# Kernel tuning notes

Hardware: AMD Instinct MI355X
Metric: run time of the kernel (lower is better)

## Reference

```python
import jax, jax.numpy as jnp
import numpy as np

B, K, D, H, L = 128, 128, 768, 8, 4
HD = D // H
FF = 4 * D
SIM = D // 4
BOOST = 0.3
SCALE = HD ** -0.5
EPS = 1e-5


def _ln(x, g, b):
    m = x.mean(-1, keepdims=True)
    v = ((x - m) ** 2).mean(-1, keepdims=True)
    return (x - m) * jax.lax.rsqrt(v + EPS) * g + b


def setup_inputs() -> dict:
    key = jax.random.key(0)
    ks = jax.random.split(key, 10)
    def n(k, shape, s=0.02):
        return jax.random.normal(k, shape, dtype=jnp.float32) * s
    return {
        'slots': jax.random.normal(ks[0], (B, K, D), dtype=jnp.float32),
        'pos_emb': n(ks[1], (1, K, D)),
        'Wq': n(ks[2], (L, D, D)),
        'Wk': n(ks[3], (L, D, D)),
        'Wv': n(ks[4], (L, D, D)),
        'Wo': n(ks[5], (L, D, D)),
        'bo': jnp.zeros((L, D), jnp.float32),
        'Wsim': n(ks[6], (L, D, SIM)),
        'g1': jnp.ones((L, D), jnp.float32),
        'b1': jnp.zeros((L, D), jnp.float32),
        'g2': jnp.ones((L, D), jnp.float32),
        'b2': jnp.zeros((L, D), jnp.float32),
        'Wff1': n(ks[7], (L, D, FF)),
        'bff1': jnp.zeros((L, FF), jnp.float32),
        'Wff2': n(ks[8], (L, FF, D)),
        'bff2': jnp.zeros((L, D), jnp.float32),
        'gf': jnp.ones((D,), jnp.float32),
        'bf': jnp.zeros((D,), jnp.float32),
    }


def reference(slots, pos_emb, Wq, Wk, Wv, Wo, bo, Wsim, g1, b1, g2, b2,
              Wff1, bff1, Wff2, bff2, gf, bf):
    x = slots + pos_emb  # K == max_slots -> full pos table
    for l in range(L):
        # --- similarity-biased multi-head self-attention (pre-norm) ---
        nx = _ln(x, g1[l], b1[l])
        q = (nx @ Wq[l]).reshape(B, K, H, HD)
        k = (nx @ Wk[l]).reshape(B, K, H, HD)
        v = (nx @ Wv[l]).reshape(B, K, H, HD)
        scores = jnp.einsum('bqhd,bkhd->bhqk', q, k) * SCALE  # [B,H,K,K]
        s = nx @ Wsim[l]  # [B,K,D/4]
        s = s / jnp.maximum(jnp.linalg.norm(s, axis=-1, keepdims=True), 1e-12)
        sim = jnp.einsum('bqc,bkc->bqk', s, s)  # cosine similarity matrix
        scores = scores + BOOST * sim[:, None, :, :]
        a = jax.nn.softmax(scores, axis=-1)
        o = jnp.einsum('bhqk,bkhd->bqhd', a, v).reshape(B, K, D)
        x = x + (o @ Wo[l] + bo[l])
        # --- feed-forward (pre-norm) ---
        nx = _ln(x, g2[l], b2[l])
        h = jax.nn.gelu(nx @ Wff1[l] + bff1[l], approximate=False)
        x = x + (h @ Wff2[l] + bff2[l])
    return _ln(x, gf, bf)
```

## Files before the change

kernel.cpp:

```cpp
#include <hip/hip_runtime.h>

typedef unsigned short u16;
typedef unsigned int u32;
typedef float f32x4 __attribute__((ext_vector_type(4)));
typedef __bf16 bf16x8 __attribute__((ext_vector_type(8)));

static constexpr int D = 768, FFD = 3072, SIMC = 192, NH = 8, HD = 96;
static constexpr int B = 128, K = 128, M = B * K, NL = 4;
static constexpr int QKVW = 2560;
static constexpr int SIMOFF = 2304;
static constexpr float QSCALE = 0.14724502f;
static constexpr float SBOOST2 = 0.6578821f;
static constexpr float EPS_F = 1e-5f;

__device__ __forceinline__ float bf2f(u16 u) {
  union { u32 i; float f; } v; v.i = ((u32)u) << 16; return v.f;
}
__device__ __forceinline__ u16 f2bf(float f) {
  union { float f; u32 i; } v; v.f = f;
  u32 u = v.i;
  u32 r = (u + 0x7FFFu + ((u >> 16) & 1u)) >> 16;
  return (u16)r;
}

__device__ __forceinline__ float fast_gelu(float x) {
  float u2 = x * (2.3020585f + 0.102944f * x * x);
  float e = __builtin_amdgcn_exp2f(u2);
  float r = __builtin_amdgcn_rcpf(1.0f + e);
  return x - x * r;
}

__device__ __forceinline__ void gload16(const void* g, void* l) {
  __builtin_amdgcn_global_load_lds(
      (const __attribute__((address_space(1))) void*)g,
      (__attribute__((address_space(3))) void*)l, 16, 0, 0);
}

__global__ __launch_bounds__(256) void addpos_kernel(
    const float* __restrict__ slots, const float* __restrict__ pos,
    u16* __restrict__ x) {
  int i = blockIdx.x * 256 + threadIdx.x;
  int m = i / D;
  int d = i - m * D;
  x[i] = f2bf(slots[i] + pos[(m & (K - 1)) * D + d]);
}

__device__ __forceinline__ float block_sum(float v, float* sbuf) {
#pragma unroll
  for (int off = 32; off > 0; off >>= 1) v += __shfl_xor(v, off, 64);
  int lane = threadIdx.x & 63, w = threadIdx.x >> 6;
  if (lane == 0) sbuf[w] = v;
  __syncthreads();
  v = sbuf[0] + sbuf[1] + sbuf[2] + sbuf[3];
  __syncthreads();
  return v;
}

template <bool OUT_BF16>
__global__ __launch_bounds__(256) void ln_kernel(
    const u16* __restrict__ x, const float* __restrict__ g,
    const float* __restrict__ b, void* __restrict__ out) {
  __shared__ float sbuf[4];
  int row = blockIdx.x, tid = threadIdx.x;
  const u16* xr = x + (size_t)row * D;
  float v0 = bf2f(xr[tid]), v1 = bf2f(xr[tid + 256]), v2 = bf2f(xr[tid + 512]);
  float s = block_sum(v0 + v1 + v2, sbuf);
  float mean = s * (1.0f / D);
  float d0 = v0 - mean, d1 = v1 - mean, d2 = v2 - mean;
  float sq = block_sum(d0 * d0 + d1 * d1 + d2 * d2, sbuf);
  float rs = rsqrtf(sq * (1.0f / D) + EPS_F);
  float y0 = d0 * rs * g[tid] + b[tid];
  float y1 = d1 * rs * g[tid + 256] + b[tid + 256];
  float y2 = d2 * rs * g[tid + 512] + b[tid + 512];
  if (OUT_BF16) {
    u16* o = (u16*)out + (size_t)row * D;
    o[tid] = f2bf(y0); o[tid + 256] = f2bf(y1); o[tid + 512] = f2bf(y2);
  } else {
    float* o = (float*)out + (size_t)row * D;
    o[tid] = y0; o[tid + 256] = y1; o[tid + 512] = y2;
  }
}

struct WAll {
  const float *wq, *wk, *wv, *wo, *wsim, *wff1, *wff2;
  u16 *tA, *tB, *tC, *tD;
};
__global__ __launch_bounds__(256) void wconv_all_kernel(WAll p, float qscale) {
  __shared__ u16 t[32][33];
  int bid = blockIdx.x;
  const float* W; u16* Wt; int N, Kd, n0, k0;
  float sc = 1.0f;
  if (bid < 2304) {
    int z = bid / 576, rem = bid - z * 576;
    W = z == 0 ? p.wq : z == 1 ? p.wk : z == 2 ? p.wv : p.wo;
    Wt = z == 0 ? p.tA : z == 1 ? p.tA + 768 * 768
       : z == 2 ? p.tA + 2 * 768 * 768 : p.tB;
    if (z == 0) sc = qscale;
    N = 768; Kd = 768;
    n0 = (rem % 24) * 32; k0 = (rem / 24) * 32;
  } else if (bid < 2448) {
    int rem = bid - 2304;
    W = p.wsim; Wt = p.tA + (size_t)SIMOFF * 768; N = SIMC; Kd = 768;
    n0 = (rem % 6) * 32; k0 = (rem / 6) * 32;
  } else if (bid < 4752) {
    int rem = bid - 2448;
    W = p.wff1; Wt = p.tC; N = FFD; Kd = 768;
    n0 = (rem % 96) * 32; k0 = (rem / 96) * 32;
  } else {
    int rem = bid - 4752;
    W = p.wff2; Wt = p.tD; N = 768; Kd = FFD;
    n0 = (rem % 24) * 32; k0 = (rem / 24) * 32;
  }
  int tid = threadIdx.x;
  int c = tid & 31, r4 = tid >> 5;
#pragma unroll
  for (int i = 0; i < 4; ++i) {
    int r = r4 + i * 8;
    t[r][c] = f2bf(W[(size_t)(k0 + r) * N + n0 + c] * sc);
  }
  __syncthreads();
#pragma unroll
  for (int i = 0; i < 4; ++i) {
    int r = r4 + i * 8;
    Wt[(size_t)(n0 + r) * Kd + k0 + c] = t[c][r];
  }
}

template <bool OUT_BF16, bool BIAS, bool GELU_, bool RESID>
__global__ __launch_bounds__(512, 2) void gemm256_kernel(
    const u16* __restrict__ A, const u16* __restrict__ Bt,
    const float* __restrict__ bias, const u16* __restrict__ resid,
    void* __restrict__ Cout, int N, int Kdim, int NBX) {
  __shared__ u16 lds[65536];
  int tid = threadIdx.x;
  int w = tid >> 6, lane = tid & 63;
  int wm = w >> 2, wn = w & 3;
  int lr = lane & 15, lg = lane >> 4;

  int nwg = gridDim.x;
  int cpx = nwg >> 3;
  int swz = (blockIdx.x & 7) * cpx + (blockIdx.x >> 3);
  int bx = swz % NBX, by = swz / NBX;
  int n0 = bx << 8, m0 = by << 8;

  int scol = ((lane & 7) ^ (lane >> 3)) << 3;
  size_t aOff = (size_t)((w << 4) + (lane >> 3)) * Kdim + scol;
  u16* ldsU = lds;

  auto stageA = [&](int buf, int h, int t) {
    const u16* g = A + (size_t)(m0 + (h << 7)) * Kdim + ((size_t)t << 6) + aOff;
    u16* l = ldsU + buf * 32768 + h * 8192 + (w << 10);
    gload16(g, l);
    gload16(g + ((size_t)Kdim << 3), l + 512);
  };
  auto stageB = [&](int buf, int h, int t) {
    const u16* g = Bt + (size_t)(n0 + (h << 7)) * Kdim + ((size_t)t << 6) + aOff;
    u16* l = ldsU + buf * 32768 + 16384 + h * 8192 + (w << 10);
    gload16(g, l);
    gload16(g + ((size_t)Kdim << 3), l + 512);
  };

  const u16* lA0p = ldsU;
  const u16* lB0p = ldsU + 16384;
  const u16* lA1p = ldsU + 32768;
  const u16* lB1p = ldsU + 49152;
  int arow = (wm * 128 + lr) * 64;
  int brow = (wn * 64 + lr) * 64;
  int swz0 = (((lg * 16)) ^ ((lr & 7) << 4)) >> 1;
  int swz1 = ((64 + lg * 16) ^ ((lr & 7) << 4)) >> 1;

  f32x4 acc[8][4] = {};
  bf16x8 ar[2][4], br[2][4];

#define READ_A_KS(BASE, MSEG, KS)                                            \
  do {                                                                       \
    _Pragma("unroll") for (int mm = 0; mm < 4; ++mm) {                       \
      const u16* p_ = (BASE) + arow + ((MSEG) * 64 + mm * 16) * 64;          \
      ar[KS][mm] = *(const bf16x8*)(p_ + ((KS) ? swz1 : swz0));              \
    }                                                                        \
  } while (0)
#define READ_B_KS(BASE, NSEG, KS)                                            \
  do {                                                                       \
    _Pragma("unroll") for (int nn = 0; nn < 2; ++nn) {                       \
      const u16* p_ = (BASE) + brow + ((NSEG) * 32 + nn * 16) * 64;          \
      br[KS][(NSEG) * 2 + nn] = *(const bf16x8*)(p_ + ((KS) ? swz1 : swz0)); \
    }                                                                        \
  } while (0)
#define MFMA_Q(MSEG, NSEG)                                                   \
  do {                                                                       \
    __builtin_amdgcn_s_setprio(1);                                           \
    _Pragma("unroll") for (int ks = 0; ks < 2; ++ks)                         \
      _Pragma("unroll") for (int mm = 0; mm < 4; ++mm)                       \
        _Pragma("unroll") for (int nn = 0; nn < 2; ++nn)                     \
          acc[(MSEG) * 4 + mm][(NSEG) * 2 + nn] =                            \
              __builtin_amdgcn_mfma_f32_16x16x32_bf16(                       \
                  ar[ks][mm], br[ks][(NSEG) * 2 + nn],                       \
                  acc[(MSEG) * 4 + mm][(NSEG) * 2 + nn], 0, 0, 0);           \
    __builtin_amdgcn_s_setprio(0);                                           \
  } while (0)
#define PSYNC()                                                              \
  do {                                                                       \
    __builtin_amdgcn_sched_barrier(0);                                       \
    asm volatile("s_waitcnt lgkmcnt(0)" ::: "memory");                       \
    __builtin_amdgcn_s_barrier();                                            \
    __builtin_amdgcn_sched_barrier(0);                                       \
  } while (0)
#define PSYNC_V(N)                                                           \
  do {                                                                       \
    __builtin_amdgcn_sched_barrier(0);                                       \
    asm volatile("s_waitcnt vmcnt(" #N ") lgkmcnt(0)" ::: "memory");         \
    __builtin_amdgcn_s_barrier();                                            \
    __builtin_amdgcn_sched_barrier(0);                                       \
  } while (0)

  int NK = Kdim >> 6, NI = NK >> 1;
  stageA(0, 0, 0); stageA(0, 1, 0); stageB(0, 0, 0); stageB(0, 1, 0);
  stageB(1, 0, 1); stageB(1, 1, 1);
  asm volatile("s_waitcnt vmcnt(4)" ::: "memory");
  __builtin_amdgcn_s_barrier();
  __builtin_amdgcn_sched_barrier(0);

  for (int i = 0; i < NI; ++i) {
    int t1 = 2 * i + 1, t2 = 2 * i + 2, t3 = 2 * i + 3;
    bool last = (i == NI - 1);
    stageA(1, 0, t1);
    READ_A_KS(lA0p, 0, 0); READ_B_KS(lB0p, 0, 0);
    READ_A_KS(lA0p, 0, 1); READ_B_KS(lB0p, 0, 1);
    MFMA_Q(0, 0);
    PSYNC();
    stageA(1, 1, t1);
    READ_B_KS(lB0p, 1, 0); READ_B_KS(lB0p, 1, 1);
    MFMA_Q(0, 1);
    PSYNC();
    if (!last) { stageB(0, 0, t2); stageB(0, 1, t2); }
    READ_A_KS(lA0p, 1, 0); READ_A_KS(lA0p, 1, 1);
    MFMA_Q(1, 0); MFMA_Q(1, 1);
    if (last) PSYNC_V(0);
    else      PSYNC_V(4);
    if (!last) stageA(0, 0, t2);
    READ_A_KS(lA1p, 0, 0); READ_B_KS(lB1p, 0, 0);
    READ_A_KS(lA1p, 0, 1); READ_B_KS(lB1p, 0, 1);
    MFMA_Q(0, 0);
    PSYNC();
    if (!last) stageA(0, 1, t2);
    READ_B_KS(lB1p, 1, 0); READ_B_KS(lB1p, 1, 1);
    MFMA_Q(0, 1);
    PSYNC();
    if (!last) { stageB(1, 0, t3); stageB(1, 1, t3); }
    READ_A_KS(lA1p, 1, 0); READ_A_KS(lA1p, 1, 1);
    MFMA_Q(1, 0); MFMA_Q(1, 1);
    if (last) PSYNC();
    else      PSYNC_V(4);
  }

#pragma unroll
  for (int m = 0; m < 8; ++m) {
#pragma unroll
    for (int n = 0; n < 4; ++n) {
      int col = n0 + wn * 64 + n * 16 + lr;
      float bv = BIAS ? bias[col] : 0.0f;
#pragma unroll
      for (int r = 0; r < 4; ++r) {
        int row = m0 + wm * 128 + m * 16 + lg * 4 + r;
        float v = acc[m][n][r];
        if (BIAS) v += bv;
        if (GELU_) v = fast_gelu(v);
        if (RESID) v += bf2f(resid[(size_t)row * N + col]);
        if (OUT_BF16) ((u16*)Cout)[(size_t)row * N + col] = f2bf(v);
        else ((float*)Cout)[(size_t)row * N + col] = v;
      }
    }
  }
#undef READ_A_KS
#undef READ_B_KS
#undef MFMA_Q
#undef PSYNC
#undef PSYNC_V
}

__global__ __launch_bounds__(256) void simpre_kernel(
    const u16* __restrict__ qkvb, u16* __restrict__ psim) {
  __shared__ u16 sln[128][200];
  int b = blockIdx.x, tid = threadIdx.x;
  {
    int row = tid >> 1, half = tid & 1;
    const u16* sr = qkvb + ((size_t)(b * K + row)) * QKVW + SIMOFF + half * 96;
    u16 v[96];
    float sq = 0.f;
#pragma unroll
    for (int j = 0; j < 12; ++j) {
      uint4 u4 = *(const uint4*)(sr + j * 8);
      u32 uu[4] = {u4.x, u4.y, u4.z, u4.w};
#pragma unroll
      for (int t = 0; t < 4; ++t) {
        v[j * 8 + 2 * t] = (u16)(uu[t] & 0xffffu);
        v[j * 8 + 2 * t + 1] = (u16)(uu[t] >> 16);
      }
    }
#pragma unroll
    for (int j = 0; j < 96; ++j) { float f = bf2f(v[j]); sq += f * f; }
    sq += __shfl_xor(sq, 1, 64);
    float inv = SBOOST2 / fmaxf(sqrtf(sq), 1e-12f);
#pragma unroll
    for (int j = 0; j < 96; ++j) sln[row][half * 96 + j] = f2bf(bf2f(v[j]) * inv);
  }
  __syncthreads();
  int w = tid >> 6, lane = tid & 63;
  int lr = lane & 15, lg = lane >> 4;
  int q0 = 32 * w;
  f32x4 accs[2][8] = {};
#pragma unroll
  for (int ks = 0; ks < 6; ++ks) {
    bf16x8 af[2];
#pragma unroll
    for (int m = 0; m < 2; ++m)
      af[m] = *(const bf16x8*)(&sln[q0 + 16 * m + lr][ks * 32 + lg * 8]);
#pragma unroll
    for (int n = 0; n < 8; ++n) {
      bf16x8 bf = *(const bf16x8*)(&sln[16 * n + lr][ks * 32 + lg * 8]);
#pragma unroll
      for (int m = 0; m < 2; ++m)
        accs[m][n] = __builtin_amdgcn_mfma_f32_16x16x32_bf16(af[m], bf, accs[m][n], 0, 0, 0);
    }
  }
  u16* pb = psim + (size_t)b * K * K;
#pragma unroll
  for (int m = 0; m < 2; ++m)
#pragma unroll
    for (int n = 0; n < 8; ++n)
#pragma unroll
      for (int r = 0; r < 4; ++r)
        pb[(size_t)(q0 + 16 * m + 4 * lg + r) * K + 16 * n + lr] = f2bf(accs[m][n][r]);
}

__global__ __launch_bounds__(256) void attn_kernel(
    const u16* __restrict__ qkv, const u16* __restrict__ psim,
    u16* __restrict__ ob) {
  __shared__ u16 Vt[96][136];
  __shared__ u16 Pl[4][32][136];
  int bh = blockIdx.x, b = bh >> 3, h = bh & 7;
  int tid = threadIdx.x, w = tid >> 6, lane = tid & 63;
  int lr = lane & 15, lg = lane >> 4;
  const u16* qb = qkv + (size_t)b * K * QKVW + h * HD;
  const u16* kb = qb + D;
  const u16* vb = qb + 2 * D;
  for (int idx = tid; idx < 128 * 12; idx += 256) {
    int r = idx / 12, db = idx - r * 12;
    uint4 v4 = *(const uint4*)(vb + (size_t)r * QKVW + db * 8);
    u32 vv[4] = {v4.x, v4.y, v4.z, v4.w};
#pragma unroll
    for (int j = 0; j < 4; ++j) {
      Vt[db * 8 + 2 * j][r] = (u16)(vv[j] & 0xffffu);
      Vt[db * 8 + 2 * j + 1][r] = (u16)(vv[j] >> 16);
    }
  }
  u16* siml = &Pl[0][0][0];
  {
    const u16* pb = psim + (size_t)b * K * K;
    for (int c = tid; c < 2048; c += 256) {
      int r = c >> 4, cc = c & 15;
      *(uint4*)(siml + r * 136 + cc * 8) = *(const uint4*)(pb + r * 128 + cc * 8);
    }
  }
  __syncthreads();
  int q0 = 32 * w;
  f32x4 accs[2][8];
#pragma unroll
  for (int m = 0; m < 2; ++m)
#pragma unroll
    for (int n = 0; n < 8; ++n)
#pragma unroll
      for (int r = 0; r < 4; ++r)
        accs[m][n][r] = bf2f(siml[(q0 + 16 * m + 4 * lg + r) * 136 + 16 * n + lr]);
#pragma unroll
  for (int ks = 0; ks < 3; ++ks) {
    bf16x8 af[2];
#pragma unroll
    for (int m = 0; m < 2; ++m)
      af[m] = *(const bf16x8*)(qb + (size_t)(q0 + 16 * m + lr) * QKVW + ks * 32 + lg * 8);
#pragma unroll
    for (int n = 0; n < 8; ++n) {
      bf16x8 bf = *(const bf16x8*)(kb + (size_t)(16 * n + lr) * QKVW + ks * 32 + lg * 8);
#pragma unroll
      for (int m = 0; m < 2; ++m)
        accs[m][n] = __builtin_amdgcn_mfma_f32_16x16x32_bf16(af[m], bf, accs[m][n], 0, 0, 0);
    }
  }
#pragma unroll
  for (int m = 0; m < 2; ++m) {
    float mx[4] = {-3e38f, -3e38f, -3e38f, -3e38f};
#pragma unroll
    for (int n = 0; n < 8; ++n)
#pragma unroll
      for (int r = 0; r < 4; ++r) mx[r] = fmaxf(mx[r], accs[m][n][r]);
#pragma unroll
    for (int r = 0; r < 4; ++r) {
      mx[r] = fmaxf(mx[r], __shfl_xor(mx[r], 1, 64));
      mx[r] = fmaxf(mx[r], __shfl_xor(mx[r], 2, 64));
      mx[r] = fmaxf(mx[r], __shfl_xor(mx[r], 4, 64));
      mx[r] = fmaxf(mx[r], __shfl_xor(mx[r], 8, 64));
    }
    float sm[4] = {0.f, 0.f, 0.f, 0.f};
#pragma unroll
    for (int n = 0; n < 8; ++n)
#pragma unroll
      for (int r = 0; r < 4; ++r) {
        float e = __builtin_amdgcn_exp2f(accs[m][n][r] - mx[r]);
        accs[m][n][r] = e;
        sm[r] += e;
      }
#pragma unroll
    for (int r = 0; r < 4; ++r) {
      sm[r] += __shfl_xor(sm[r], 1, 64);
      sm[r] += __shfl_xor(sm[r], 2, 64);
      sm[r] += __shfl_xor(sm[r], 4, 64);
      sm[r] += __shfl_xor(sm[r], 8, 64);
    }
    float inv[4];
#pragma unroll
    for (int r = 0; r < 4; ++r) inv[r] = 1.0f / sm[r];
#pragma unroll
    for (int n = 0; n < 8; ++n)
#pragma unroll
      for (int r = 0; r < 4; ++r)
        Pl[w][16 * m + 4 * lg + r][16 * n + lr] = f2bf(accs[m][n][r] * inv[r]);
  }
  __syncthreads();
  f32x4 acco[2][6] = {};
#pragma unroll
  for (int ks = 0; ks < 4; ++ks) {
    bf16x8 pa[2];
#pragma unroll
    for (int m = 0; m < 2; ++m)
      pa[m] = *(const bf16x8*)(&Pl[w][16 * m + lr][ks * 32 + lg * 8]);
#pragma unroll
    for (int n = 0; n < 6; ++n) {
      bf16x8 bv = *(const bf16x8*)(&Vt[16 * n + lr][ks * 32 + lg * 8]);
#pragma unroll
      for (int m = 0; m < 2; ++m)
        acco[m][n] = __builtin_amdgcn_mfma_f32_16x16x32_bf16(pa[m], bv, acco[m][n], 0, 0, 0);
    }
  }
  u16* obb = ob + (size_t)b * K * D + h * HD;
#pragma unroll
  for (int m = 0; m < 2; ++m)
#pragma unroll
    for (int n = 0; n < 6; ++n)
#pragma unroll
      for (int r = 0; r < 4; ++r)
        obb[(size_t)(q0 + 16 * m + 4 * lg + r) * D + 16 * n + lr] = f2bf(acco[m][n][r]);
}

extern "C" void kernel_launch(void* const* d_in, const int* in_sizes, int n_in,
                              void* d_out, int out_size, void* d_ws, size_t ws_size,
                              hipStream_t stream) {
  (void)in_sizes; (void)n_in; (void)out_size;
  const float* slots = (const float*)d_in[0];
  const float* pos   = (const float*)d_in[1];
  const float* Wq    = (const float*)d_in[2];
  const float* Wk    = (const float*)d_in[3];
  const float* Wv    = (const float*)d_in[4];
  const float* Wo    = (const float*)d_in[5];
  const float* bo    = (const float*)d_in[6];
  const float* Wsim  = (const float*)d_in[7];
  const float* g1    = (const float*)d_in[8];
  const float* b1    = (const float*)d_in[9];
  const float* g2    = (const float*)d_in[10];
  const float* b2    = (const float*)d_in[11];
  const float* Wff1  = (const float*)d_in[12];
  const float* bff1  = (const float*)d_in[13];
  const float* Wff2  = (const float*)d_in[14];
  const float* bff2  = (const float*)d_in[15];
  const float* gf    = (const float*)d_in[16];
  const float* bfin  = (const float*)d_in[17];

  char* p = (char*)d_ws;
  u16*   x    = (u16*)p;   p += (size_t)M * D * 2;
  u16*   nx   = (u16*)p;   p += (size_t)M * D * 2;
  u16*   qkvb = (u16*)p;   p += (size_t)M * QKVW * 2;
  u16*   ob   = (u16*)p;   p += (size_t)M * D * 2;
  u16*   psim = (u16*)p;   p += (size_t)B * K * K * 2;
  u16*   wtA  = (u16*)p;   p += (size_t)QKVW * D * 2;
  u16*   wtB  = (u16*)p;   p += (size_t)D * D * 2;
  u16*   wtC  = (u16*)p;   p += (size_t)FFD * D * 2;
  u16*   wtD  = (u16*)p;   p += (size_t)D * FFD * 2;
  if ((size_t)(p - (char*)d_ws) > ws_size) return;
  u16* hb = qkvb;

  addpos_kernel<<<M * D / 256, 256, 0, stream>>>(slots, pos, x);

  int nbx_qkv = QKVW / 256, nwg_qkv = nbx_qkv * (M / 256);
  int nbx_o   = D / 256,    nwg_o   = nbx_o * (M / 256);
  int nbx_f1  = FFD / 256,  nwg_f1  = nbx_f1 * (M / 256);

  for (int l = 0; l < NL; ++l) {
    ln_kernel<true><<<M, 256, 0, stream>>>(x, g1 + l * D, b1 + l * D, nx);
    WAll wp = {Wq + (size_t)l * D * D, Wk + (size_t)l * D * D,
               Wv + (size_t)l * D * D, Wo + (size_t)l * D * D,
               Wsim + (size_t)l * D * SIMC,
               Wff1 + (size_t)l * D * FFD, Wff2 + (size_t)l * FFD * D,
               wtA, wtB, wtC, wtD};
    wconv_all_kernel<<<7056, 256, 0, stream>>>(wp, QSCALE);
    gemm256_kernel<true, false, false, false><<<nwg_qkv, 512, 0, stream>>>(
        nx, wtA, nullptr, nullptr, qkvb, QKVW, D, nbx_qkv);
    simpre_kernel<<<B, 256, 0, stream>>>(qkvb, psim);
    attn_kernel<<<B * NH, 256, 0, stream>>>(qkvb, psim, ob);
    gemm256_kernel<true, true, false, true><<<nwg_o, 512, 0, stream>>>(
        ob, wtB, bo + l * D, x, x, D, D, nbx_o);
    ln_kernel<true><<<M, 256, 0, stream>>>(x, g2 + l * D, b2 + l * D, nx);
    gemm256_kernel<true, true, true, false><<<nwg_f1, 512, 0, stream>>>(
        nx, wtC, bff1 + l * FFD, nullptr, hb, FFD, D, nbx_f1);
    gemm256_kernel<true, true, false, true><<<nwg_o, 512, 0, stream>>>(
        hb, wtD, bff2 + l * D, x, x, D, FFD, nbx_o);
  }
  ln_kernel<false><<<M, 256, 0, stream>>>(x, gf, bfin, d_out);
}
```

Measured before the change: 1.402 ms.

## Fold LayerNorm into GEMM epilogue and convert all layer weights once

Replaces the per-layer LayerNorm kernel, which wrote a normalized bf16 activation, with a stats-only kernel that stores per-row mean and rstd. The gamma scale is folded into the bf16 weights, and precomputed column sums of gamma*W and beta*W let the GEMM epilogue apply the normalization, so the GEMM reads the raw residual stream directly. Weight conversion for all four layers is also merged into one launch before the loop, which needs a larger workspace. Subtracting mean times colsum after a bf16 GEMM on un-centered inputs can lose precision through cancellation.

```diff
diff --git a/kernel.cpp b/kernel.cpp
--- a/kernel.cpp
+++ b/kernel.cpp
@@ -56,10 +56,25 @@
   return v;
 }
 
-template <bool OUT_BF16>
+__global__ __launch_bounds__(256) void stats_kernel(
+    const u16* __restrict__ x, float* __restrict__ mu, float* __restrict__ rr) {
+  __shared__ float sbuf[4];
+  int row = blockIdx.x, tid = threadIdx.x;
+  const u16* xr = x + (size_t)row * D;
+  float v0 = bf2f(xr[tid]), v1 = bf2f(xr[tid + 256]), v2 = bf2f(xr[tid + 512]);
+  float s = block_sum(v0 + v1 + v2, sbuf);
+  float mean = s * (1.0f / D);
+  float d0 = v0 - mean, d1 = v1 - mean, d2 = v2 - mean;
+  float sq = block_sum(d0 * d0 + d1 * d1 + d2 * d2, sbuf);
+  if (tid == 0) {
+    mu[row] = mean;
+    rr[row] = rsqrtf(sq * (1.0f / D) + EPS_F);
+  }
+}
+
 __global__ __launch_bounds__(256) void ln_kernel(
     const u16* __restrict__ x, const float* __restrict__ g,
-    const float* __restrict__ b, void* __restrict__ out) {
+    const float* __restrict__ b, float* __restrict__ out) {
   __shared__ float sbuf[4];
   int row = blockIdx.x, tid = threadIdx.x;
   const u16* xr = x + (size_t)row * D;
@@ -69,68 +84,118 @@
   float d0 = v0 - mean, d1 = v1 - mean, d2 = v2 - mean;
   float sq = block_sum(d0 * d0 + d1 * d1 + d2 * d2, sbuf);
   float rs = rsqrtf(sq * (1.0f / D) + EPS_F);
-  float y0 = d0 * rs * g[tid] + b[tid];
-  float y1 = d1 * rs * g[tid + 256] + b[tid + 256];
-  float y2 = d2 * rs * g[tid + 512] + b[tid + 512];
-  if (OUT_BF16) {
-    u16* o = (u16*)out + (size_t)row * D;
-    o[tid] = f2bf(y0); o[tid + 256] = f2bf(y1); o[tid + 512] = f2bf(y2);
+  float* o = out + (size_t)row * D;
+  o[tid] = d0 * rs * g[tid] + b[tid];
+  o[tid + 256] = d1 * rs * g[tid + 256] + b[tid + 256];
+  o[tid + 512] = d2 * rs * g[tid + 512] + b[tid + 512];
+}
+
+struct WAll4 {
+  const float *wq, *wk, *wv, *wo, *wsim, *wff1, *wff2;
+  const float *g1, *b1, *g2, *b2;
+  u16 *tA, *tB, *tC, *tD;
+  float* wgwb;
+};
+__global__ __launch_bounds__(256) void wconv_all_kernel(WAll4 p) {
+  __shared__ u16 t[32][33];
+  __shared__ float pg[8][33], pb[8][33];
+  int bid = blockIdx.x, tid = threadIdx.x;
+  int c = tid & 31, r4 = tid >> 5;
+  if (bid < 28224) {
+    int l = bid / 7056, b = bid - l * 7056;
+    const float* W; u16* Wt; int N, Kd, n0, k0;
+    const float* gk = nullptr;
+    float sc = 1.0f;
+    if (b < 2304) {
+      int z = b / 576, rem = b - z * 576;
+      N = 768; Kd = 768;
+      n0 = (rem % 24) * 32; k0 = (rem / 24) * 32;
+      if (z == 0) { W = p.wq + (size_t)l * 589824; Wt = p.tA + (size_t)l * 1966080; sc = QSCALE; gk = p.g1 + l * 768; }
+      else if (z == 1) { W = p.wk + (size_t)l * 589824; Wt = p.tA + (size_t)l * 1966080 + 589824; gk = p.g1 + l * 768; }
+      else if (z == 2) { W = p.wv + (size_t)l * 589824; Wt = p.tA + (size_t)l * 1966080 + 1179648; gk = p.g1 + l * 768; }
+      else { W = p.wo + (size_t)l * 589824; Wt = p.tB + (size_t)l * 589824; }
+    } else if (b < 2448) {
+      int rem = b - 2304;
+      W = p.wsim + (size_t)l * 147456;
+      Wt = p.tA + (size_t)l * 1966080 + (size_t)SIMOFF * 768;
+      N = SIMC; Kd = 768;
+      n0 = (rem % 6) * 32; k0 = (rem / 6) * 32;
+      gk = p.g1 + l * 768;
+    } else if (b < 4752) {
+      int rem = b - 2448;
+      W = p.wff1 + (size_t)l * 2359296; Wt = p.tC + (size_t)l * 2359296;
+      N = FFD; Kd = 768;
+      n0 = (rem % 96) * 32; k0 = (rem / 96) * 32;
+      gk = p.g2 + l * 768;
+    } else {
+      int rem = b - 4752;
+      W = p.wff2 + (size_t)l * 2359296; Wt = p.tD + (size_t)l * 2359296;
+      N = 768; Kd = FFD;
+      n0 = (rem % 24) * 32; k0 = (rem / 24) * 32;
+    }
+#pragma unroll
+    for (int i = 0; i < 4; ++i) {
+      int r = r4 + i * 8, k = k0 + r;
+      float gv = gk ? gk[k] : 1.0f;
+      t[r][c] = f2bf(W[(size_t)k * N + n0 + c] * gv * sc);
+    }
+    __syncthreads();
+#pragma unroll
+    for (int i = 0; i < 4; ++i) {
+      int r = r4 + i * 8;
+      Wt[(size_t)(n0 + r) * Kd + k0 + c] = t[c][r];
+    }
+    return;
+  }
+  int rem2 = bid - 28224;
+  int l = rem2 / 176, t2 = rem2 - l * 176;
+  float* wgwbL = p.wgwb + l * 11264;
+  const float* W; const float* gk; const float* bk;
+  int N2, coff, colbase;
+  float sc2 = 1.0f;
+  float* wgp; float* wbp;
+  if (t2 < 80) {
+    colbase = t2 * 32;
+    wgp = wgwbL; wbp = wgwbL + 2560;
+    gk = p.g1 + l * 768; bk = p.b1 + l * 768;
+    if (colbase < 768) { W = p.wq + (size_t)l * 589824; N2 = 768; coff = colbase; sc2 = QSCALE; }
+    else if (colbase < 1536) { W = p.wk + (size_t)l * 589824; N2 = 768; coff = colbase - 768; }
+    else if (colbase < 2304) { W = p.wv + (size_t)l * 589824; N2 = 768; coff = colbase - 1536; }
+    else if (colbase < 2496) { W = p.wsim + (size_t)l * 147456; N2 = SIMC; coff = colbase - 2304; }
+    else {
+      if (tid < 32) { wgp[colbase + tid] = 0.f; wbp[colbase + tid] = 0.f; }
+      return;
+    }
   } else {
-    float* o = (float*)out + (size_t)row * D;
-    o[tid] = y0; o[tid + 256] = y1; o[tid + 512] = y2;
-  }
-}
-
-struct WAll {
-  const float *wq, *wk, *wv, *wo, *wsim, *wff1, *wff2;
-  u16 *tA, *tB, *tC, *tD;
-};
-__global__ __launch_bounds__(256) void wconv_all_kernel(WAll p, float qscale) {
-  __shared__ u16 t[32][33];
-  int bid = blockIdx.x;
-  const float* W; u16* Wt; int N, Kd, n0, k0;
-  float sc = 1.0f;
-  if (bid < 2304) {
-    int z = bid / 576, rem = bid - z * 576;
-    W = z == 0 ? p.wq : z == 1 ? p.wk : z == 2 ? p.wv : p.wo;
-    Wt = z == 0 ? p.tA : z == 1 ? p.tA + 768 * 768
-       : z == 2 ? p.tA + 2 * 768 * 768 : p.tB;
-    if (z == 0) sc = qscale;
-    N = 768; Kd = 768;
-    n0 = (rem % 24) * 32; k0 = (rem / 24) * 32;
-  } else if (bid < 2448) {
-    int rem = bid - 2304;
-    W = p.wsim; Wt = p.tA + (size_t)SIMOFF * 768; N = SIMC; Kd = 768;
-    n0 = (rem % 6) * 32; k0 = (rem / 6) * 32;
-  } else if (bid < 4752) {
-    int rem = bid - 2448;
-    W = p.wff1; Wt = p.tC; N = FFD; Kd = 768;
-    n0 = (rem % 96) * 32; k0 = (rem / 96) * 32;
-  } else {
-    int rem = bid - 4752;
-    W = p.wff2; Wt = p.tD; N = 768; Kd = FFD;
-    n0 = (rem % 24) * 32; k0 = (rem / 24) * 32;
-  }
-  int tid = threadIdx.x;
-  int c = tid & 31, r4 = tid >> 5;
-#pragma unroll
-  for (int i = 0; i < 4; ++i) {
-    int r = r4 + i * 8;
-    t[r][c] = f2bf(W[(size_t)(k0 + r) * N + n0 + c] * sc);
-  }
+    colbase = (t2 - 80) * 32;
+    wgp = wgwbL + 5120; wbp = wgwbL + 8192;
+    gk = p.g2 + l * 768; bk = p.b2 + l * 768;
+    W = p.wff1 + (size_t)l * 2359296; N2 = FFD; coff = colbase;
+  }
+  float swg = 0.f, swb = 0.f;
+  for (int k = r4; k < 768; k += 8) {
+    float val = W[(size_t)k * N2 + coff + c] * sc2;
+    swg += gk[k] * val;
+    swb += bk[k] * val;
+  }
+  pg[r4][c] = swg; pb[r4][c] = swb;
   __syncthreads();
-#pragma unroll
-  for (int i = 0; i < 4; ++i) {
-    int r = r4 + i * 8;
-    Wt[(size_t)(n0 + r) * Kd + k0 + c] = t[c][r];
-  }
-}
-
-template <bool OUT_BF16, bool BIAS, bool GELU_, bool RESID>
+  if (tid < 32) {
+    float a = 0.f, bb = 0.f;
+#pragma unroll
+    for (int j = 0; j < 8; ++j) { a += pg[j][tid]; bb += pb[j][tid]; }
+    wgp[colbase + tid] = a;
+    wbp[colbase + tid] = bb;
+  }
+}
+
+template <bool BIAS, bool GELU_, bool RESID, bool LNFOLD>
 __global__ __launch_bounds__(512, 2) void gemm256_kernel(
     const u16* __restrict__ A, const u16* __restrict__ Bt,
     const float* __restrict__ bias, const u16* __restrict__ resid,
-    void* __restrict__ Cout, int N, int Kdim, int NBX) {
+    u16* __restrict__ Cout, int N, int Kdim, int NBX,
+    const float* __restrict__ mu, const float* __restrict__ rr,
+    const float* __restrict__ wg, const float* __restrict__ wb) {
   __shared__ u16 lds[65536];
   int tid = threadIdx.x;
   int w = tid >> 6, lane = tid & 63;
@@ -255,19 +320,29 @@
 
 #pragma unroll
   for (int m = 0; m < 8; ++m) {
+    float muv[4], rrv[4];
+    if (LNFOLD) {
+#pragma unroll
+      for (int r = 0; r < 4; ++r) {
+        int row = m0 + wm * 128 + m * 16 + lg * 4 + r;
+        muv[r] = mu[row]; rrv[r] = rr[row];
+      }
+    }
 #pragma unroll
     for (int n = 0; n < 4; ++n) {
       int col = n0 + wn * 64 + n * 16 + lr;
+      float wgc = LNFOLD ? wg[col] : 0.0f;
+      float wbc = LNFOLD ? wb[col] : 0.0f;
       float bv = BIAS ? bias[col] : 0.0f;
 #pragma unroll
       for (int r = 0; r < 4; ++r) {
         int row = m0 + wm * 128 + m * 16 + lg * 4 + r;
         float v = acc[m][n][r];
+        if (LNFOLD) v = rrv[r] * (v - muv[r] * wgc) + wbc;
         if (BIAS) v += bv;
         if (GELU_) v = fast_gelu(v);
         if (RESID) v += bf2f(resid[(size_t)row * N + col]);
-        if (OUT_BF16) ((u16*)Cout)[(size_t)row * N + col] = f2bf(v);
-        else ((float*)Cout)[(size_t)row * N + col] = v;
+        Cout[(size_t)row * N + col] = f2bf(v);
       }
     }
   }
@@ -476,42 +551,46 @@
 
   char* p = (char*)d_ws;
   u16*   x    = (u16*)p;   p += (size_t)M * D * 2;
-  u16*   nx   = (u16*)p;   p += (size_t)M * D * 2;
   u16*   qkvb = (u16*)p;   p += (size_t)M * QKVW * 2;
   u16*   ob   = (u16*)p;   p += (size_t)M * D * 2;
   u16*   psim = (u16*)p;   p += (size_t)B * K * K * 2;
-  u16*   wtA  = (u16*)p;   p += (size_t)QKVW * D * 2;
-  u16*   wtB  = (u16*)p;   p += (size_t)D * D * 2;
-  u16*   wtC  = (u16*)p;   p += (size_t)FFD * D * 2;
-  u16*   wtD  = (u16*)p;   p += (size_t)D * FFD * 2;
+  float* mu   = (float*)p; p += (size_t)M * 4;
+  float* rr   = (float*)p; p += (size_t)M * 4;
+  u16*   wtA4 = (u16*)p;   p += (size_t)4 * QKVW * D * 2;
+  u16*   wtB4 = (u16*)p;   p += (size_t)4 * D * D * 2;
+  u16*   wtC4 = (u16*)p;   p += (size_t)4 * FFD * D * 2;
+  u16*   wtD4 = (u16*)p;   p += (size_t)4 * D * FFD * 2;
+  float* wgwb = (float*)p; p += (size_t)4 * 11264 * 4;
   if ((size_t)(p - (char*)d_ws) > ws_size) return;
   u16* hb = qkvb;
 
   addpos_kernel<<<M * D / 256, 256, 0, stream>>>(slots, pos, x);
+  WAll4 wp = {Wq, Wk, Wv, Wo, Wsim, Wff1, Wff2, g1, b1, g2, b2,
+              wtA4, wtB4, wtC4, wtD4, wgwb};
+  wconv_all_kernel<<<28224 + 704, 256, 0, stream>>>(wp);
 
   int nbx_qkv = QKVW / 256, nwg_qkv = nbx_qkv * (M / 256);
   int nbx_o   = D / 256,    nwg_o   = nbx_o * (M / 256);
   int nbx_f1  = FFD / 256,  nwg_f1  = nbx_f1 * (M / 256);
 
   for (int l = 0; l < NL; ++l) {
-    ln_kernel<true><<<M, 256, 0, stream>>>(x, g1 + l * D, b1 + l * D, nx);
-    WAll wp = {Wq + (size_t)l * D * D, Wk + (size_t)l * D * D,
-               Wv + (size_t)l * D * D, Wo + (size_t)l * D * D,
-               Wsim + (size_t)l * D * SIMC,
-               Wff1 + (size_t)l * D * FFD, Wff2 + (size_t)l * FFD * D,
-               wtA, wtB, wtC, wtD};
-    wconv_all_kernel<<<7056, 256, 0, stream>>>(wp, QSCALE);
-    gemm256_kernel<true, false, false, false><<<nwg_qkv, 512, 0, stream>>>(
-        nx, wtA, nullptr, nullptr, qkvb, QKVW, D, nbx_qkv);
+    float* wgwbL = wgwb + l * 11264;
+    stats_kernel<<<M, 256, 0, stream>>>(x, mu, rr);
+    gemm256_kernel<false, false, false, true><<<nwg_qkv, 512, 0, stream>>>(
+        x, wtA4 + (size_t)l * QKVW * D, nullptr, nullptr, qkvb, QKVW, D, nbx_qkv,
+        mu, rr, wgwbL, wgwbL + 2560);
     simpre_kernel<<<B, 256, 0, stream>>>(qkvb, psim);
     attn_kernel<<<B * NH, 256, 0, stream>>>(qkvb, psim, ob);
-    gemm256_kernel<true, true, false, true><<<nwg_o, 512, 0, stream>>>(
-        ob, wtB, bo + l * D, x, x, D, D, nbx_o);
-    ln_kernel<true><<<M, 256, 0, stream>>>(x, g2 + l * D, b2 + l * D, nx);
-    gemm256_kernel<true, true, true, false><<<nwg_f1, 512, 0, stream>>>(
-        nx, wtC, bff1 + l * FFD, nullptr, hb, FFD, D, nbx_f1);
-    gemm256_kernel<true, true, false, true><<<nwg_o, 512, 0, stream>>>(
-        hb, wtD, bff2 + l * D, x, x, D, FFD, nbx_o);
-  }
-  ln_kernel<false><<<M, 256, 0, stream>>>(x, gf, bfin, d_out);
-}
+    gemm256_kernel<true, false, true, false><<<nwg_o, 512, 0, stream>>>(
+        ob, wtB4 + (size_t)l * D * D, bo + l * D, x, x, D, D, nbx_o,
+        nullptr, nullptr, nullptr, nullptr);
+    stats_kernel<<<M, 256, 0, stream>>>(x, mu, rr);
+    gemm256_kernel<true, true, false, true><<<nwg_f1, 512, 0, stream>>>(
+        x, wtC4 + (size_t)l * FFD * D, bff1 + l * FFD, nullptr, hb, FFD, D, nbx_f1,
+        mu, rr, wgwbL + 5120, wgwbL + 8192);
+    gemm256_kernel<true, false, true, false><<<nwg_o, 512, 0, stream>>>(
+        hb, wtD4 + (size_t)l * D * FFD, bff2 + l * D, x, x, D, FFD, nbx_o,
+        nullptr, nullptr, nullptr, nullptr);
+  }
+  ln_kernel<<<M, 256, 0, stream>>>(x, gf, bfin, (float*)d_out);
+}
```

Result: slower. 1.439 ms (+2.6%).

## Batch weight conversion for all layers into one launch and regroup GEMM LDS reads

Applied to the files above, without the earlier changes.

Weight transpose/bf16 conversion for all four layers now runs in a single large kernel before the layer loop, writing into per-layer slices of an enlarged workspace, instead of one conversion launch per layer. This removes three launches and lets the conversion saturate the GPU once. The GEMM main loop also issues both A-half stages together and groups B fragment reads so that two MFMA quarters run per barrier, dropping one barrier per half-iteration. The OUT_BF16 template parameter is removed as cleanup. The cost is a larger workspace footprint and higher register and LDS-read pressure per phase.

```diff
diff --git a/kernel.cpp b/kernel.cpp
--- a/kernel.cpp
+++ b/kernel.cpp
@@ -88,27 +88,32 @@
 __global__ __launch_bounds__(256) void wconv_all_kernel(WAll p, float qscale) {
   __shared__ u16 t[32][33];
   int bid = blockIdx.x;
+  int l = bid / 7056, b = bid - l * 7056;
   const float* W; u16* Wt; int N, Kd, n0, k0;
   float sc = 1.0f;
-  if (bid < 2304) {
-    int z = bid / 576, rem = bid - z * 576;
-    W = z == 0 ? p.wq : z == 1 ? p.wk : z == 2 ? p.wv : p.wo;
-    Wt = z == 0 ? p.tA : z == 1 ? p.tA + 768 * 768
-       : z == 2 ? p.tA + 2 * 768 * 768 : p.tB;
-    if (z == 0) sc = qscale;
+  if (b < 2304) {
+    int z = b / 576, rem = b - z * 576;
     N = 768; Kd = 768;
     n0 = (rem % 24) * 32; k0 = (rem / 24) * 32;
-  } else if (bid < 2448) {
-    int rem = bid - 2304;
-    W = p.wsim; Wt = p.tA + (size_t)SIMOFF * 768; N = SIMC; Kd = 768;
+    if (z == 0) { W = p.wq + (size_t)l * 589824; Wt = p.tA + (size_t)l * 1966080; sc = qscale; }
+    else if (z == 1) { W = p.wk + (size_t)l * 589824; Wt = p.tA + (size_t)l * 1966080 + 589824; }
+    else if (z == 2) { W = p.wv + (size_t)l * 589824; Wt = p.tA + (size_t)l * 1966080 + 1179648; }
+    else { W = p.wo + (size_t)l * 589824; Wt = p.tB + (size_t)l * 589824; }
+  } else if (b < 2448) {
+    int rem = b - 2304;
+    W = p.wsim + (size_t)l * 147456;
+    Wt = p.tA + (size_t)l * 1966080 + (size_t)SIMOFF * 768;
+    N = SIMC; Kd = 768;
     n0 = (rem % 6) * 32; k0 = (rem / 6) * 32;
-  } else if (bid < 4752) {
-    int rem = bid - 2448;
-    W = p.wff1; Wt = p.tC; N = FFD; Kd = 768;
+  } else if (b < 4752) {
+    int rem = b - 2448;
+    W = p.wff1 + (size_t)l * 2359296; Wt = p.tC + (size_t)l * 2359296;
+    N = FFD; Kd = 768;
     n0 = (rem % 96) * 32; k0 = (rem / 96) * 32;
   } else {
-    int rem = bid - 4752;
-    W = p.wff2; Wt = p.tD; N = 768; Kd = FFD;
+    int rem = b - 4752;
+    W = p.wff2 + (size_t)l * 2359296; Wt = p.tD + (size_t)l * 2359296;
+    N = 768; Kd = FFD;
     n0 = (rem % 24) * 32; k0 = (rem / 24) * 32;
   }
   int tid = threadIdx.x;
@@ -126,11 +131,11 @@
   }
 }
 
-template <bool OUT_BF16, bool BIAS, bool GELU_, bool RESID>
+template <bool BIAS, bool GELU_, bool RESID>
 __global__ __launch_bounds__(512, 2) void gemm256_kernel(
     const u16* __restrict__ A, const u16* __restrict__ Bt,
     const float* __restrict__ bias, const u16* __restrict__ resid,
-    void* __restrict__ Cout, int N, int Kdim, int NBX) {
+    u16* __restrict__ Cout, int N, int Kdim, int NBX) {
   __shared__ u16 lds[65536];
   int tid = threadIdx.x;
   int w = tid >> 6, lane = tid & 63;
@@ -223,28 +228,20 @@
   for (int i = 0; i < NI; ++i) {
     int t1 = 2 * i + 1, t2 = 2 * i + 2, t3 = 2 * i + 3;
     bool last = (i == NI - 1);
-    stageA(1, 0, t1);
-    READ_A_KS(lA0p, 0, 0); READ_B_KS(lB0p, 0, 0);
-    READ_A_KS(lA0p, 0, 1); READ_B_KS(lB0p, 0, 1);
-    MFMA_Q(0, 0);
-    PSYNC();
-    stageA(1, 1, t1);
-    READ_B_KS(lB0p, 1, 0); READ_B_KS(lB0p, 1, 1);
-    MFMA_Q(0, 1);
+    stageA(1, 0, t1); stageA(1, 1, t1);
+    READ_A_KS(lA0p, 0, 0); READ_B_KS(lB0p, 0, 0); READ_B_KS(lB0p, 1, 0);
+    READ_A_KS(lA0p, 0, 1); READ_B_KS(lB0p, 0, 1); READ_B_KS(lB0p, 1, 1);
+    MFMA_Q(0, 0); MFMA_Q(0, 1);
     PSYNC();
     if (!last) { stageB(0, 0, t2); stageB(0, 1, t2); }
     READ_A_KS(lA0p, 1, 0); READ_A_KS(lA0p, 1, 1);
     MFMA_Q(1, 0); MFMA_Q(1, 1);
     if (last) PSYNC_V(0);
     else      PSYNC_V(4);
-    if (!last) stageA(0, 0, t2);
-    READ_A_KS(lA1p, 0, 0); READ_B_KS(lB1p, 0, 0);
-    READ_A_KS(lA1p, 0, 1); READ_B_KS(lB1p, 0, 1);
-    MFMA_Q(0, 0);
-    PSYNC();
-    if (!last) stageA(0, 1, t2);
-    READ_B_KS(lB1p, 1, 0); READ_B_KS(lB1p, 1, 1);
-    MFMA_Q(0, 1);
+    if (!last) { stageA(0, 0, t2); stageA(0, 1, t2); }
+    READ_A_KS(lA1p, 0, 0); READ_B_KS(lB1p, 0, 0); READ_B_KS(lB1p, 1, 0);
+    READ_A_KS(lA1p, 0, 1); READ_B_KS(lB1p, 0, 1); READ_B_KS(lB1p, 1, 1);
+    MFMA_Q(0, 0); MFMA_Q(0, 1);
     PSYNC();
     if (!last) { stageB(1, 0, t3); stageB(1, 1, t3); }
     READ_A_KS(lA1p, 1, 0); READ_A_KS(lA1p, 1, 1);
@@ -266,8 +263,7 @@
         if (BIAS) v += bv;
         if (GELU_) v = fast_gelu(v);
         if (RESID) v += bf2f(resid[(size_t)row * N + col]);
-        if (OUT_BF16) ((u16*)Cout)[(size_t)row * N + col] = f2bf(v);
-        else ((float*)Cout)[(size_t)row * N + col] = v;
+        Cout[(size_t)row * N + col] = f2bf(v);
       }
     }
   }
@@ -480,14 +476,16 @@
   u16*   qkvb = (u16*)p;   p += (size_t)M * QKVW * 2;
   u16*   ob   = (u16*)p;   p += (size_t)M * D * 2;
   u16*   psim = (u16*)p;   p += (size_t)B * K * K * 2;
-  u16*   wtA  = (u16*)p;   p += (size_t)QKVW * D * 2;
-  u16*   wtB  = (u16*)p;   p += (size_t)D * D * 2;
-  u16*   wtC  = (u16*)p;   p += (size_t)FFD * D * 2;
-  u16*   wtD  = (u16*)p;   p += (size_t)D * FFD * 2;
+  u16*   wtA4 = (u16*)p;   p += (size_t)4 * QKVW * D * 2;
+  u16*   wtB4 = (u16*)p;   p += (size_t)4 * D * D * 2;
+  u16*   wtC4 = (u16*)p;   p += (size_t)4 * FFD * D * 2;
+  u16*   wtD4 = (u16*)p;   p += (size_t)4 * D * FFD * 2;
   if ((size_t)(p - (char*)d_ws) > ws_size) return;
   u16* hb = qkvb;
 
   addpos_kernel<<<M * D / 256, 256, 0, stream>>>(slots, pos, x);
+  WAll wp = {Wq, Wk, Wv, Wo, Wsim, Wff1, Wff2, wtA4, wtB4, wtC4, wtD4};
+  wconv_all_kernel<<<28224, 256, 0, stream>>>(wp, QSCALE);
 
   int nbx_qkv = QKVW / 256, nwg_qkv = nbx_qkv * (M / 256);
   int nbx_o   = D / 256,    nwg_o   = nbx_o * (M / 256);
@@ -495,23 +493,17 @@
 
   for (int l = 0; l < NL; ++l) {
     ln_kernel<true><<<M, 256, 0, stream>>>(x, g1 + l * D, b1 + l * D, nx);
-    WAll wp = {Wq + (size_t)l * D * D, Wk + (size_t)l * D * D,
-               Wv + (size_t)l * D * D, Wo + (size_t)l * D * D,
-               Wsim + (size_t)l * D * SIMC,
-               Wff1 + (size_t)l * D * FFD, Wff2 + (size_t)l * FFD * D,
-               wtA, wtB, wtC, wtD};
-    wconv_all_kernel<<<7056, 256, 0, stream>>>(wp, QSCALE);
-    gemm256_kernel<true, false, false, false><<<nwg_qkv, 512, 0, stream>>>(
-        nx, wtA, nullptr, nullptr, qkvb, QKVW, D, nbx_qkv);
+    gemm256_kernel<false, false, false><<<nwg_qkv, 512, 0, stream>>>(
+        nx, wtA4 + (size_t)l * QKVW * D, nullptr, nullptr, qkvb, QKVW, D, nbx_qkv);
     simpre_kernel<<<B, 256, 0, stream>>>(qkvb, psim);
     attn_kernel<<<B * NH, 256, 0, stream>>>(qkvb, psim, ob);
-    gemm256_kernel<true, true, false, true><<<nwg_o, 512, 0, stream>>>(
-        ob, wtB, bo + l * D, x, x, D, D, nbx_o);
+    gemm256_kernel<true, false, true><<<nwg_o, 512, 0, stream>>>(
+        ob, wtB4 + (size_t)l * D * D, bo + l * D, x, x, D, D, nbx_o);
     ln_kernel<true><<<M, 256, 0, stream>>>(x, g2 + l * D, b2 + l * D, nx);
-    gemm256_kernel<true, true, true, false><<<nwg_f1, 512, 0, stream>>>(
-        nx, wtC, bff1 + l * FFD, nullptr, hb, FFD, D, nbx_f1);
-    gemm256_kernel<true, true, false, true><<<nwg_o, 512, 0, stream>>>(
-        hb, wtD, bff2 + l * D, x, x, D, FFD, nbx_o);
+    gemm256_kernel<true, true, false><<<nwg_f1, 512, 0, stream>>>(
+        nx, wtC4 + (size_t)l * FFD * D, bff1 + l * FFD, nullptr, hb, FFD, D, nbx_f1);
+    gemm256_kernel<true, false, true><<<nwg_o, 512, 0, stream>>>(
+        hb, wtD4 + (size_t)l * D * FFD, bff2 + l * D, x, x, D, FFD, nbx_o);
   }
   ln_kernel<false><<<M, 256, 0, stream>>>(x, gf, bfin, d_out);
 }
```

After: 1.395 ms. Within noise of the previous version (-0.5%).
